# Kernel optimization log

Measured on AMD Instinct MI355X. Metric: run time of the kernel, lower is better.

The kernel has to match this reference:

```python
import jax, jax.numpy as jnp
import numpy as np

B, S, E, H = 64, 512, 768, 256


def setup_inputs() -> dict:
    key = jax.random.key(0)
    ks = jax.random.split(key, 9)
    sc = 0.02  # small init so relu-activated LSTM stays numerically sane
    x = jax.random.normal(ks[0], (B, S, E), dtype=jnp.float32)
    kernel_f = jax.random.normal(ks[1], (E, 4 * H), dtype=jnp.float32) * sc
    rec_f = jax.random.normal(ks[2], (H, 4 * H), dtype=jnp.float32) * sc
    bias_f = jnp.zeros((4 * H,), dtype=jnp.float32)
    kernel_b = jax.random.normal(ks[3], (E, 4 * H), dtype=jnp.float32) * sc
    rec_b = jax.random.normal(ks[4], (H, 4 * H), dtype=jnp.float32) * sc
    bias_b = jnp.zeros((4 * H,), dtype=jnp.float32)
    Wd = jax.random.normal(ks[5], (S * H, 2), dtype=jnp.float32) * sc
    bd = jnp.zeros((2,), dtype=jnp.float32)
    return {"x": x, "kernel_f": kernel_f, "rec_f": rec_f, "bias_f": bias_f,
            "kernel_b": kernel_b, "rec_b": rec_b, "bias_b": bias_b,
            "Wd": Wd, "bd": bd}


def _lstm_relu(x, kernel, rec, bias):
    # Keras LSTM with activation='relu', recurrent_activation='sigmoid'.
    # Gate order in keras kernel: [i, f, c, o].
    b, h = x.shape[0], rec.shape[0]
    xz = jnp.einsum('bse,eg->bsg', x, kernel) + bias  # [B,S,4H] precomputed input part

    def step(carry, zt):
        hp, cp = carry
        z = zt + hp @ rec  # [B,4H]
        zi, zf, zc, zo = jnp.split(z, 4, axis=-1)
        i = jax.nn.sigmoid(zi)
        f = jax.nn.sigmoid(zf)
        o = jax.nn.sigmoid(zo)
        c = f * cp + i * jax.nn.relu(zc)
        hn = o * jax.nn.relu(c)
        return (hn, c), hn

    init = (jnp.zeros((b, h), x.dtype), jnp.zeros((b, h), x.dtype))
    _, hs = jax.lax.scan(step, init, jnp.swapaxes(xz, 0, 1))  # [S,B,H]
    return jnp.swapaxes(hs, 0, 1)  # [B,S,H]


def reference(x, kernel_f, rec_f, bias_f, kernel_b, rec_b, bias_b, Wd, bd):
    h_fwd = _lstm_relu(x, kernel_f, rec_f, bias_f)
    # backward direction: process reversed sequence, reverse output back, then merge_mode='sum'
    h_bwd = _lstm_relu(x[:, ::-1], kernel_b, rec_b, bias_b)[:, ::-1]
    h = h_fwd + h_bwd  # [B,S,H]
    # dropout is identity at inference (training=None)
    flat = h.reshape(h.shape[0], -1)  # [B, S*H]
    logits = flat @ Wd + bd  # [B,2]
    return logits
```

## Files before the change

### kernel.cpp

```cpp
#include <hip/hip_runtime.h>
#include <hip/hip_bf16.h>
#include <hip/hip_fp16.h>

#define B_ 64
#define S_ 512
#define E_ 768
#define H_ 256
#define G_ 1024
#define MROWS 32768

typedef float f32x4 __attribute__((ext_vector_type(4)));
typedef float f32x16 __attribute__((ext_vector_type(16)));
typedef short short8 __attribute__((ext_vector_type(8)));
typedef _Float16 v2h __attribute__((ext_vector_type(2)));
typedef unsigned int u32x4 __attribute__((ext_vector_type(4)));


__global__ void cast_x_kernel(const float* __restrict__ x, __hip_bfloat16* __restrict__ xbf, int n) {
    int i = (blockIdx.x * 256 + threadIdx.x) * 4;
    if (i >= n) return;
    float4 v = *(const float4*)(x + i);
    xbf[i + 0] = __float2bfloat16(v.x);
    xbf[i + 1] = __float2bfloat16(v.y);
    xbf[i + 2] = __float2bfloat16(v.z);
    xbf[i + 3] = __float2bfloat16(v.w);
}

__global__ void prep_kT_kernel(const float* __restrict__ kf, const float* __restrict__ kb,
                               __hip_bfloat16* __restrict__ kT) {
    int idx = blockIdx.x * 256 + threadIdx.x;
    int dir = blockIdx.y;
    const float* src = dir ? kb : kf;
    int k = idx >> 10;
    int n = idx & 1023;
    float v = src[idx];
    kT[(size_t)dir * G_ * E_ + (size_t)n * E_ + k] = __float2bfloat16(v);
}

__global__ void prep_recQ_kernel(const float* __restrict__ rf, const float* __restrict__ rb,
                                 unsigned int* __restrict__ recQ) {
    int idx = blockIdx.x * 256 + threadIdx.x;
    int dir = blockIdx.y;
    const float* src = dir ? rb : rf;
    int g  = idx & 1023;
    int u  = (idx >> 10) & 3;
    int kk = idx >> 12;
    int k0 = 8 * kk + 2 * u;
    float a = src[(size_t)k0 * G_ + g];
    float b = src[(size_t)(k0 + 1) * G_ + g];
    v2h p;
    p[0] = (_Float16)a;
    p[1] = (_Float16)b;
    recQ[(size_t)dir * 131072 + (size_t)kk * 4096 + g * 4 + u] = __builtin_bit_cast(unsigned int, p);
}

#define TM 128
#define TN 128
#define BK 32
#define LDA 40

__global__ __launch_bounds__(256) void gemm_xz_kernel(
        const __hip_bfloat16* __restrict__ xbf,
        const __hip_bfloat16* __restrict__ kT,
        const float* __restrict__ bias_f, const float* __restrict__ bias_b,
        __hip_bfloat16* __restrict__ xz) {
    int dir  = blockIdx.z;
    int nblk = blockIdx.x;
    int mblk = blockIdx.y;
    int tid  = threadIdx.x;
    int wave = tid >> 6, lane = tid & 63;

    __shared__ __hip_bfloat16 shA[TM * LDA];
    __shared__ __hip_bfloat16 shB[TN * LDA];

    int m0 = mblk * TM;
    int n0 = nblk * TN;

    int rowl0 = tid >> 2;
    int rowl1 = rowl0 + 64;
    int k8    = (tid & 3) * 8;
    int ar0 = m0 + rowl0, ar1 = m0 + rowl1;
    int sa0 = (ar0 & ~511) | (dir ? (511 - (ar0 & 511)) : (ar0 & 511));
    int sa1 = (ar1 & ~511) | (dir ? (511 - (ar1 & 511)) : (ar1 & 511));
    const __hip_bfloat16* kbase = kT + (size_t)dir * G_ * E_;

    f32x16 acc[4] = {};

    int lm = lane & 31;
    int kq = (lane >> 5) * 8;

    for (int k0 = 0; k0 < E_; k0 += BK) {
        __syncthreads();
        *(short8*)&shA[rowl0 * LDA + k8] = *(const short8*)(xbf + (size_t)sa0 * E_ + k0 + k8);
        *(short8*)&shA[rowl1 * LDA + k8] = *(const short8*)(xbf + (size_t)sa1 * E_ + k0 + k8);
        *(short8*)&shB[rowl0 * LDA + k8] = *(const short8*)(kbase + (size_t)(n0 + rowl0) * E_ + k0 + k8);
        *(short8*)&shB[rowl1 * LDA + k8] = *(const short8*)(kbase + (size_t)(n0 + rowl1) * E_ + k0 + k8);
        __syncthreads();

#pragma unroll
        for (int kk = 0; kk < BK; kk += 16) {
            short8 afrag = *(const short8*)&shA[(wave * 32 + lm) * LDA + kk + kq];
#pragma unroll
            for (int j = 0; j < 4; ++j) {
                short8 bfrag = *(const short8*)&shB[(j * 32 + lm) * LDA + kk + kq];
                acc[j] = __builtin_amdgcn_mfma_f32_32x32x16_bf16(afrag, bfrag, acc[j], 0, 0, 0);
            }
        }
    }

    const float* bias = dir ? bias_b : bias_f;
#pragma unroll
    for (int j = 0; j < 4; ++j) {
        int col = n0 + j * 32 + lm;
        float bv = bias[col];
#pragma unroll
        for (int reg = 0; reg < 16; ++reg) {
            int row = m0 + wave * 32 + (reg & 3) + 8 * (reg >> 2) + 4 * (lane >> 5);
            xz[((size_t)dir * MROWS + row) * G_ + col] = __float2bfloat16(acc[j][reg] + bv);
        }
    }
}

__device__ inline float dot2f16(unsigned int rbits, unsigned int hbits, float acc) {
#if __has_builtin(__builtin_amdgcn_fdot2)
    return __builtin_amdgcn_fdot2(__builtin_bit_cast(v2h, rbits),
                                  __builtin_bit_cast(v2h, hbits), acc, false);
#else
    v2h r = __builtin_bit_cast(v2h, rbits);
    v2h h = __builtin_bit_cast(v2h, hbits);
    return acc + (float)r[0] * (float)h[0] + (float)r[1] * (float)h[1];
#endif
}

__device__ inline float sigmoidf(float x) { return 1.f / (1.f + __expf(-x)); }

#define KKREG 24
#define KKLDS 8
__global__ __launch_bounds__(512) void scan_kernel(
        const __hip_bfloat16* __restrict__ xz,
        const uint4* __restrict__ recQ,
        const float* __restrict__ Wd,
        const float* __restrict__ bd,
        float* __restrict__ out) {
    int b = blockIdx.x, dir = blockIdx.y, tid = threadIdx.x;
    __shared__ __align__(16) uint4 sh_rec[KKLDS * G_];
    __shared__ __align__(16) _Float16 sh_h[2][H_];
    __shared__ float rbuf[16];

    int w = tid >> 6, lane = tid & 63, lm = lane & 31, hi = lane >> 5;
    int col = w * 32 + lm;
    int g0  = col + hi * 512;
    int g1  = g0 + 256;

    const uint4* rqbase = recQ + (size_t)dir * 32768;

    u32x4 rr0[KKREG], rr1[KKREG];
    {
        unsigned long long a0 = (unsigned long long)(const void*)(rqbase + g0);
        unsigned long long a1 = (unsigned long long)(const void*)(rqbase + g1);
#pragma unroll
        for (int kk = 0; kk < KKREG; ++kk) {
            unsigned long long ka0 = a0 + (unsigned long long)kk * 16384ull;
            unsigned long long ka1 = a1 + (unsigned long long)kk * 16384ull;
            asm volatile("global_load_dwordx4 %0, %1, off" : "=v"(rr0[kk]) : "v"(ka0));
            asm volatile("global_load_dwordx4 %0, %1, off" : "=v"(rr1[kk]) : "v"(ka1));
        }
        asm volatile("s_waitcnt vmcnt(0)" ::: "memory");
    }

#pragma unroll
    for (int j = 0; j < KKLDS * 2; ++j)
        sh_rec[j * 512 + tid] = rqbase[KKREG * 1024 + j * 512 + tid];

    if (tid < H_) sh_h[0][tid] = (_Float16)0.f;
    float c = 0.f, pl0 = 0.f, pl1 = 0.f;
    float wsel = hi ? 0.f : 1.f;
    const __hip_bfloat16* xrb = xz + ((size_t)dir * MROWS + (size_t)b * S_) * G_;
    __syncthreads();

    float nxz0 = __bfloat162float(xrb[g0]);
    float nxz1 = __bfloat162float(xrb[g1]);
    int t0i = dir ? (S_ - 1) : 0;
    float2 nwv = ((const float2*)Wd)[t0i * H_ + col];

    int p = 0;
    for (int s = 0; s < S_; ++s) {
        float xz0 = nxz0, xz1 = nxz1;
        float2 wv = nwv;

        int sn = (s + 1 < S_) ? (s + 1) : (S_ - 1);
        int tn = dir ? (S_ - 1 - sn) : sn;
        nxz0 = __bfloat162float(xrb[(size_t)sn * G_ + g0]);
        nxz1 = __bfloat162float(xrb[(size_t)sn * G_ + g1]);
        nwv  = ((const float2*)Wd)[tn * H_ + col];

        const uint4* hp = (const uint4*)&sh_h[p][0];
        float z0a = 0.f, z0b = 0.f, z1a = 0.f, z1b = 0.f;

#pragma unroll
        for (int kk = 0; kk < KKREG; ++kk) {
            uint4 hv = hp[kk];
            u32x4 r0 = rr0[kk];
            u32x4 r1 = rr1[kk];
            z0a = dot2f16(r0.x, hv.x, z0a); z0b = dot2f16(r0.y, hv.y, z0b);
            z0a = dot2f16(r0.z, hv.z, z0a); z0b = dot2f16(r0.w, hv.w, z0b);
            z1a = dot2f16(r1.x, hv.x, z1a); z1b = dot2f16(r1.y, hv.y, z1b);
            z1a = dot2f16(r1.z, hv.z, z1a); z1b = dot2f16(r1.w, hv.w, z1b);
        }
#pragma unroll
        for (int j = 0; j < KKLDS; ++j) {
            uint4 hv = hp[KKREG + j];
            uint4 r0 = sh_rec[j * 1024 + g0];
            uint4 r1 = sh_rec[j * 1024 + g1];
            z0a = dot2f16(r0.x, hv.x, z0a); z0b = dot2f16(r0.y, hv.y, z0b);
            z0a = dot2f16(r0.z, hv.z, z0a); z0b = dot2f16(r0.w, hv.w, z0b);
            z1a = dot2f16(r1.x, hv.x, z1a); z1b = dot2f16(r1.y, hv.y, z1b);
            z1a = dot2f16(r1.z, hv.z, z1a); z1b = dot2f16(r1.w, hv.w, z1b);
        }

        float z0 = z0a + z0b + xz0;
        float z1 = z1a + z1b + xz1;

        float zx0 = __shfl_xor(z0, 32);
        float zx1 = __shfl_xor(z1, 32);
        float zi = hi ? zx0 : z0;
        float zf = hi ? zx1 : z1;
        float zc = hi ? z0 : zx0;
        float zo = hi ? z1 : zx1;

        float ig = sigmoidf(zi);
        float fg = sigmoidf(zf);
        float og = sigmoidf(zo);
        float cc = fmaxf(zc, 0.f);
        c = fg * c + ig * cc;
        float h = og * fmaxf(c, 0.f);
        if (hi == 0) sh_h[p ^ 1][col] = (_Float16)h;

        pl0 = fmaf(h, wv.x * wsel, pl0);
        pl1 = fmaf(h, wv.y * wsel, pl1);

        __syncthreads();
        p ^= 1;
    }

#pragma unroll
    for (int off = 32; off > 0; off >>= 1) {
        pl0 += __shfl_down(pl0, off);
        pl1 += __shfl_down(pl1, off);
    }
    if (lane == 0) {
        rbuf[w] = pl0; rbuf[8 + w] = pl1;
    }
    __syncthreads();
    if (tid == 0) {
        float t0 = 0.f, t1 = 0.f;
#pragma unroll
        for (int i = 0; i < 8; ++i) { t0 += rbuf[i]; t1 += rbuf[8 + i]; }
        atomicAdd(&out[b * 2 + 0], t0);
        atomicAdd(&out[b * 2 + 1], t1);
    }
    if (dir == 0 && tid < 2) atomicAdd(&out[b * 2 + tid], bd[tid]);
}

extern "C" void kernel_launch(void* const* d_in, const int* in_sizes, int n_in,
                              void* d_out, int out_size, void* d_ws, size_t ws_size,
                              hipStream_t stream) {
    const float* x        = (const float*)d_in[0];
    const float* kernel_f = (const float*)d_in[1];
    const float* rec_f    = (const float*)d_in[2];
    const float* bias_f   = (const float*)d_in[3];
    const float* kernel_b = (const float*)d_in[4];
    const float* rec_b    = (const float*)d_in[5];
    const float* bias_b   = (const float*)d_in[6];
    const float* Wd       = (const float*)d_in[7];
    const float* bd       = (const float*)d_in[8];
    float* out = (float*)d_out;

    char* w = (char*)d_ws;
    __hip_bfloat16* xz  = (__hip_bfloat16*)w;
    __hip_bfloat16* xbf = (__hip_bfloat16*)(w + 134217728);
    __hip_bfloat16* kT  = (__hip_bfloat16*)(w + 184549376);
    unsigned int*  recQ = (unsigned int*) (w + 187695104);

    int nx = B_ * S_ * E_;
    cast_x_kernel<<<nx / (256 * 4), 256, 0, stream>>>(x, xbf, nx);
    prep_kT_kernel<<<dim3((E_ * G_) / 256, 2), 256, 0, stream>>>(kernel_f, kernel_b, kT);
    prep_recQ_kernel<<<dim3(131072 / 256, 2), 256, 0, stream>>>(rec_f, rec_b, recQ);

    gemm_xz_kernel<<<dim3(G_ / TN, MROWS / TM, 2), 256, 0, stream>>>(xbf, kT, bias_f, bias_b, xz);

    hipMemsetAsync(d_out, 0, (size_t)out_size * sizeof(float), stream);
    scan_kernel<<<dim3(B_, 2), 512, 0, stream>>>(xz, (const uint4*)recQ, Wd, bd, out);
}
```

Before: 1.145 ms.

## Load GEMM tiles via global_load_lds and remap block order across XCDs

The xz GEMM now loads A and B tiles straight from global memory into LDS with global_load_lds 16-byte transfers. This skips the register round-trip, and the padded LDS layout is dropped for an unpadded one. The grid is flattened to 1D and blocks are remapped so consecutive blocks spread across the 8 XCDs while N-tiles of the same M-tile stay grouped for L2 reuse. The unpadded layout may bring back LDS bank conflicts on the MFMA fragment reads. The GEMM is also only part of the total time, which includes the sequential scan kernel.

```diff
diff --git a/kernel.cpp b/kernel.cpp
--- a/kernel.cpp
+++ b/kernel.cpp
@@ -57,32 +57,48 @@
 #define TM 128
 #define TN 128
 #define BK 32
-#define LDA 40
+
+__device__ inline void glds16(const __hip_bfloat16* g, void* lds) {
+    __builtin_amdgcn_global_load_lds(
+        (const __attribute__((address_space(1))) unsigned int*)g,
+        (__attribute__((address_space(3))) unsigned int*)lds, 16, 0, 0);
+}
 
 __global__ __launch_bounds__(256) void gemm_xz_kernel(
         const __hip_bfloat16* __restrict__ xbf,
         const __hip_bfloat16* __restrict__ kT,
         const float* __restrict__ bias_f, const float* __restrict__ bias_b,
         __hip_bfloat16* __restrict__ xz) {
-    int dir  = blockIdx.z;
-    int nblk = blockIdx.x;
-    int mblk = blockIdx.y;
+    int p = blockIdx.x;
+    int v = (p & 7) * 512 + (p >> 3);
+    int nblk = v & 7;
+    int g    = v >> 3;
+    int mblk = g & 255;
+    int dir  = g >> 8;
     int tid  = threadIdx.x;
     int wave = tid >> 6, lane = tid & 63;
 
-    __shared__ __hip_bfloat16 shA[TM * LDA];
-    __shared__ __hip_bfloat16 shB[TN * LDA];
+    __shared__ __hip_bfloat16 shA[TM * BK];
+    __shared__ __hip_bfloat16 shB[TN * BK];
 
     int m0 = mblk * TM;
     int n0 = nblk * TN;
 
-    int rowl0 = tid >> 2;
-    int rowl1 = rowl0 + 64;
-    int k8    = (tid & 3) * 8;
-    int ar0 = m0 + rowl0, ar1 = m0 + rowl1;
+    int r0 = wave * 32 + (lane >> 2);
+    int r1 = r0 + 16;
+    int c8 = (lane & 3) * 8;
+    int ar0 = m0 + r0, ar1 = m0 + r1;
     int sa0 = (ar0 & ~511) | (dir ? (511 - (ar0 & 511)) : (ar0 & 511));
     int sa1 = (ar1 & ~511) | (dir ? (511 - (ar1 & 511)) : (ar1 & 511));
     const __hip_bfloat16* kbase = kT + (size_t)dir * G_ * E_;
+    const __hip_bfloat16* gA0 = xbf + (size_t)sa0 * E_ + c8;
+    const __hip_bfloat16* gA1 = xbf + (size_t)sa1 * E_ + c8;
+    const __hip_bfloat16* gB0 = kbase + (size_t)(n0 + r0) * E_ + c8;
+    const __hip_bfloat16* gB1 = kbase + (size_t)(n0 + r1) * E_ + c8;
+    char* lA0 = (char*)shA + wave * 2048;
+    char* lA1 = (char*)shA + wave * 2048 + 1024;
+    char* lB0 = (char*)shB + wave * 2048;
+    char* lB1 = (char*)shB + wave * 2048 + 1024;
 
     f32x16 acc[4] = {};
 
@@ -91,18 +107,18 @@
 
     for (int k0 = 0; k0 < E_; k0 += BK) {
         __syncthreads();
-        *(short8*)&shA[rowl0 * LDA + k8] = *(const short8*)(xbf + (size_t)sa0 * E_ + k0 + k8);
-        *(short8*)&shA[rowl1 * LDA + k8] = *(const short8*)(xbf + (size_t)sa1 * E_ + k0 + k8);
-        *(short8*)&shB[rowl0 * LDA + k8] = *(const short8*)(kbase + (size_t)(n0 + rowl0) * E_ + k0 + k8);
-        *(short8*)&shB[rowl1 * LDA + k8] = *(const short8*)(kbase + (size_t)(n0 + rowl1) * E_ + k0 + k8);
+        glds16(gA0 + k0, lA0);
+        glds16(gA1 + k0, lA1);
+        glds16(gB0 + k0, lB0);
+        glds16(gB1 + k0, lB1);
         __syncthreads();
 
 #pragma unroll
         for (int kk = 0; kk < BK; kk += 16) {
-            short8 afrag = *(const short8*)&shA[(wave * 32 + lm) * LDA + kk + kq];
+            short8 afrag = *(const short8*)&shA[(wave * 32 + lm) * BK + kk + kq];
 #pragma unroll
             for (int j = 0; j < 4; ++j) {
-                short8 bfrag = *(const short8*)&shB[(j * 32 + lm) * LDA + kk + kq];
+                short8 bfrag = *(const short8*)&shB[(j * 32 + lm) * BK + kk + kq];
                 acc[j] = __builtin_amdgcn_mfma_f32_32x32x16_bf16(afrag, bfrag, acc[j], 0, 0, 0);
             }
         }
@@ -287,7 +303,7 @@
     prep_kT_kernel<<<dim3((E_ * G_) / 256, 2), 256, 0, stream>>>(kernel_f, kernel_b, kT);
     prep_recQ_kernel<<<dim3(131072 / 256, 2), 256, 0, stream>>>(rec_f, rec_b, recQ);
 
-    gemm_xz_kernel<<<dim3(G_ / TN, MROWS / TM, 2), 256, 0, stream>>>(xbf, kT, bias_f, bias_b, xz);
+    gemm_xz_kernel<<<4096, 256, 0, stream>>>(xbf, kT, bias_f, bias_b, xz);
 
     hipMemsetAsync(d_out, 0, (size_t)out_size * sizeof(float), stream);
     scan_kernel<<<dim3(B_, 2), 512, 0, stream>>>(xz, (const uint4*)recQ, Wd, bd, out);
```

Result: no change. 1.129 ms (-1.5%).
